# Kernel tuning notes

Hardware: AMD Instinct MI355X
Metric: run time of the kernel (lower is better)

Reference implementation:

```python
import jax, jax.numpy as jnp
import numpy as np

B, IN, HID, LAT, EH = 32768, 512, 2048, 128, 512
MID = max(HID // 2, LAT * 2)      # 1024
HALF = max(EH // 2, 4)            # 256
EPS = 1e-5
LN10 = float(np.log(10.0))


def setup_inputs() -> dict:
    key = jax.random.key(0)
    ks = jax.random.split(key, 24)
    r = lambda k, shp, s=0.02: (jax.random.normal(k, shp, dtype=jnp.float32) * s)
    d = {
        "x": jax.random.normal(ks[0], (B, IN), dtype=jnp.float32),
        "group_idx": jax.random.randint(ks[1], (B,), 0, 3),
        # encoder: Linear(IN,HID)+BN+ELU, Linear(HID,MID)+BN+ELU, Linear(MID,LAT)
        "e_w1": r(ks[2], (HID, IN)), "e_b1": jnp.zeros((HID,), jnp.float32),
        "e_g1": jnp.ones((HID,), jnp.float32), "e_be1": jnp.zeros((HID,), jnp.float32),
        "e_w2": r(ks[3], (MID, HID)), "e_b2": jnp.zeros((MID,), jnp.float32),
        "e_g2": jnp.ones((MID,), jnp.float32), "e_be2": jnp.zeros((MID,), jnp.float32),
        "e_w3": r(ks[4], (LAT, MID)), "e_b3": jnp.zeros((LAT,), jnp.float32),
        # shared: Linear(LAT+IN,HID)+BN+ELU, Linear(HID,MID)+BN+ELU
        "s_w1": r(ks[5], (HID, LAT + IN)), "s_b1": jnp.zeros((HID,), jnp.float32),
        "s_g1": jnp.ones((HID,), jnp.float32), "s_be1": jnp.zeros((HID,), jnp.float32),
        "s_w2": r(ks[6], (MID, HID)), "s_b2": jnp.zeros((MID,), jnp.float32),
        "s_g2": jnp.ones((MID,), jnp.float32), "s_be2": jnp.zeros((MID,), jnp.float32),
        # 3 expert heads, stacked on leading axis E=3
        "h_w1": r(ks[7], (3, EH, MID)), "h_b1": jnp.zeros((3, EH), jnp.float32),
        "h_w2": r(ks[8], (3, HALF, EH)), "h_b2": jnp.zeros((3, HALF), jnp.float32),
        "h_w3": r(ks[9], (3, HALF)), "h_b3": jnp.zeros((3,), jnp.float32),
    }
    return d


def _bn(h, g, b):
    # BatchNorm1d in training mode: batch mean, biased batch var
    m = jnp.mean(h, axis=0)
    v = jnp.var(h, axis=0)
    return (h - m) * (g / jnp.sqrt(v + EPS)) + b


def _elu(h):
    return jax.nn.elu(h)


def reference(x, group_idx,
              e_w1, e_b1, e_g1, e_be1, e_w2, e_b2, e_g2, e_be2, e_w3, e_b3,
              s_w1, s_b1, s_g1, s_be1, s_w2, s_b2, s_g2, s_be2,
              h_w1, h_b1, h_w2, h_b2, h_w3, h_b3):
    # encoder
    h = _elu(_bn(x @ e_w1.T + e_b1, e_g1, e_be1))
    h = _elu(_bn(h @ e_w2.T + e_b2, e_g2, e_be2))
    latent = h @ e_w3.T + e_b3                              # [B, LAT]
    # shared trunk
    z = jnp.concatenate([latent, x], axis=-1)               # [B, LAT+IN]
    h = _elu(_bn(z @ s_w1.T + s_b1, s_g1, s_be1))
    hidden = _elu(_bn(h @ s_w2.T + s_b2, s_g2, s_be2))      # [B, MID]
    # expert heads: compute all 3 (tiny vs trunk), then select per-row group
    t1 = _elu(jnp.einsum('bm,ehm->ebh', hidden, h_w1) + h_b1[:, None, :])   # [3,B,EH]
    t2 = _elu(jnp.einsum('ebh,efh->ebf', t1, h_w2) + h_b2[:, None, :])      # [3,B,HALF]
    pred_all = jnp.einsum('ebf,ef->eb', t2, h_w3) + h_b3[:, None]           # [3,B]
    pred_raw = jnp.take_along_axis(pred_all, group_idx[None, :], axis=0)[0] # [B]
    pred_log = -jax.nn.softplus(pred_raw)
    pred_prob = jnp.exp(pred_log * jnp.float32(LN10))       # 10 ** pred_log
    return pred_log, pred_prob
```

## Files before the change

kernel.cpp:

```cpp
#include <hip/hip_runtime.h>
#include <math.h>

#define B_    32768
#define LN10_ 2.302585092994046f
#define MT_H  264
#define NBLK  128

typedef __attribute__((ext_vector_type(8))) short short8;
typedef __attribute__((ext_vector_type(4))) float f32x4;

typedef const __attribute__((address_space(1))) void gvoid_t;
typedef __attribute__((address_space(3))) void svoid_t;

__device__ __forceinline__ void gl16(const void* g, void* l) {
  __builtin_amdgcn_global_load_lds((gvoid_t*)g, (svoid_t*)l, 16, 0, 0);
}

__device__ __forceinline__ float bf2f(unsigned int u) {
  union { unsigned int i; float f; } v; v.i = u << 16; return v.f;
}
__device__ __forceinline__ unsigned short f2bf(float f) {
  union { float f; unsigned int i; } v; v.f = f;
  unsigned int x = v.i;
  unsigned int r = x + 0x7FFFu + ((x >> 16) & 1u);
  return (unsigned short)(r >> 16);
}

#define HLF 8192

__global__ __launch_bounds__(512)
void gemm256(const unsigned short* __restrict__ A0_, int lda,
             const unsigned short* __restrict__ W0_, int ldw,
             unsigned short* __restrict__ C0, int ldc, int K,
             float* __restrict__ st, int Ntot) {
  __shared__ __align__(16) unsigned short lds[65536];
  const int t = threadIdx.x;
  const int nx = gridDim.x, ny = gridDim.y;
  const int f = blockIdx.y * nx + blockIdx.x;
  const int xcd = f & 7, g = f >> 3;
  const int gdiv = g / nx;
  const int mt = xcd * (ny >> 3) + gdiv;
  const int nt = g - gdiv * nx;
  const int mBase = mt * 256, nBase = nt * 256;
  const unsigned short* Ap = A0_ + (size_t)mBase * lda;
  const unsigned short* Wp = W0_ + (size_t)nBase * ldw;
  const int w = t >> 6, l = t & 63;
  const int wr = w >> 2, wc = w & 3;
  const int lm = l & 15, lg = l >> 4;

  const int rr = t >> 3;
  const int xc = ((t & 7) ^ (rr & 7)) << 3;
  const unsigned short* gA = Ap + (size_t)rr * lda + xc;
  const unsigned short* gB = Wp + (size_t)rr * ldw + xc;

#define SG(ptr, ld, rowoff, dst) \
    gl16((ptr) + (size_t)(rowoff) * (ld) + ko_, &lds[(dst) + t * 8])
#define STAGE_A0(tt) { const int d_=((tt)&1)<<15; const size_t ko_=(size_t)(tt)*64; \
    SG(gA,lda,0,d_);          SG(gA,lda,64,d_+4096); }
#define STAGE_A1(tt) { const int d_=((tt)&1)<<15; const size_t ko_=(size_t)(tt)*64; \
    SG(gA,lda,128,d_+8192);   SG(gA,lda,192,d_+12288); }
#define STAGE_B0(tt) { const int d_=((tt)&1)<<15; const size_t ko_=(size_t)(tt)*64; \
    SG(gB,ldw,0,d_+16384);    SG(gB,ldw,64,d_+20480); }
#define STAGE_B1(tt) { const int d_=((tt)&1)<<15; const size_t ko_=(size_t)(tt)*64; \
    SG(gB,ldw,128,d_+24576);  SG(gB,ldw,192,d_+28672); }

  const int cs0 = ((lg) ^ (l & 7)) << 3;
  const int cs1 = ((4 | lg) ^ (l & 7)) << 3;

  f32x4 acc[8][4];
#pragma unroll
  for (int i = 0; i < 8; ++i)
#pragma unroll
    for (int j = 0; j < 4; ++j) {
      f32x4 z4 = {0.f, 0.f, 0.f, 0.f};
      acc[i][j] = z4;
    }

  const int NT = K >> 6;
  STAGE_A0(0); STAGE_A1(0); STAGE_B0(0); STAGE_B1(0);
  asm volatile("s_waitcnt vmcnt(2)" ::: "memory");
  __builtin_amdgcn_s_barrier();

  short8 af[8], bq[4];
  for (int tt = 0; tt < NT; ++tt) {
    const int d = (tt & 1) << 15;
    const bool more = (tt + 1 < NT);
    const int abase = d + wr * HLF + lm * 64;
    const int bbase = d + 2 * HLF + (wc * 32 + lm) * 64;
#pragma unroll
    for (int i = 0; i < 8; ++i) af[i] = *(const short8*)&lds[abase + i * 1024 + cs0];
    bq[0] = *(const short8*)&lds[bbase + cs0];
    bq[1] = *(const short8*)&lds[bbase + 1024 + cs0];
    if (more) {
      STAGE_A0(tt + 1);
      asm volatile("s_waitcnt vmcnt(2)" ::: "memory");
    } else {
      asm volatile("s_waitcnt vmcnt(0)" ::: "memory");
    }
    __builtin_amdgcn_s_barrier();
    asm volatile("s_waitcnt lgkmcnt(0)" ::: "memory");
    __builtin_amdgcn_sched_barrier(0);
    __builtin_amdgcn_s_setprio(1);
#pragma unroll
    for (int i = 0; i < 8; ++i) {
      acc[i][0] = __builtin_amdgcn_mfma_f32_16x16x32_bf16(af[i], bq[0], acc[i][0], 0, 0, 0);
      acc[i][1] = __builtin_amdgcn_mfma_f32_16x16x32_bf16(af[i], bq[1], acc[i][1], 0, 0, 0);
    }
    __builtin_amdgcn_s_setprio(0);
    __builtin_amdgcn_s_barrier();
    bq[2] = *(const short8*)&lds[bbase + HLF + cs0];
    bq[3] = *(const short8*)&lds[bbase + HLF + 1024 + cs0];
    if (more) STAGE_A1(tt + 1);
    __builtin_amdgcn_s_barrier();
    asm volatile("s_waitcnt lgkmcnt(0)" ::: "memory");
    __builtin_amdgcn_sched_barrier(0);
    __builtin_amdgcn_s_setprio(1);
#pragma unroll
    for (int i = 0; i < 8; ++i) {
      acc[i][2] = __builtin_amdgcn_mfma_f32_16x16x32_bf16(af[i], bq[2], acc[i][2], 0, 0, 0);
      acc[i][3] = __builtin_amdgcn_mfma_f32_16x16x32_bf16(af[i], bq[3], acc[i][3], 0, 0, 0);
    }
    __builtin_amdgcn_s_setprio(0);
    __builtin_amdgcn_s_barrier();
#pragma unroll
    for (int i = 0; i < 8; ++i) af[i] = *(const short8*)&lds[abase + i * 1024 + cs1];
    bq[0] = *(const short8*)&lds[bbase + cs1];
    bq[1] = *(const short8*)&lds[bbase + 1024 + cs1];
    if (more) STAGE_B0(tt + 1);
    __builtin_amdgcn_s_barrier();
    asm volatile("s_waitcnt lgkmcnt(0)" ::: "memory");
    __builtin_amdgcn_sched_barrier(0);
    __builtin_amdgcn_s_setprio(1);
#pragma unroll
    for (int i = 0; i < 8; ++i) {
      acc[i][0] = __builtin_amdgcn_mfma_f32_16x16x32_bf16(af[i], bq[0], acc[i][0], 0, 0, 0);
      acc[i][1] = __builtin_amdgcn_mfma_f32_16x16x32_bf16(af[i], bq[1], acc[i][1], 0, 0, 0);
    }
    __builtin_amdgcn_s_setprio(0);
    __builtin_amdgcn_s_barrier();
    bq[2] = *(const short8*)&lds[bbase + HLF + cs1];
    bq[3] = *(const short8*)&lds[bbase + HLF + 1024 + cs1];
    if (more) {
      STAGE_B1(tt + 1);
      asm volatile("s_waitcnt vmcnt(2)" ::: "memory");
    }
    __builtin_amdgcn_s_barrier();
    asm volatile("s_waitcnt lgkmcnt(0)" ::: "memory");
    __builtin_amdgcn_sched_barrier(0);
    __builtin_amdgcn_s_setprio(1);
#pragma unroll
    for (int i = 0; i < 8; ++i) {
      acc[i][2] = __builtin_amdgcn_mfma_f32_16x16x32_bf16(af[i], bq[2], acc[i][2], 0, 0, 0);
      acc[i][3] = __builtin_amdgcn_mfma_f32_16x16x32_bf16(af[i], bq[3], acc[i][3], 0, 0, 0);
    }
    __builtin_amdgcn_s_setprio(0);
    __builtin_amdgcn_s_barrier();
  }

#pragma unroll
  for (int j = 0; j < 4; ++j) {
    int n = nBase + (j >> 1) * 128 + wc * 32 + (j & 1) * 16 + lm;
    float s1 = 0.f, q1 = 0.f;
#pragma unroll
    for (int i = 0; i < 8; ++i) {
      int m0 = mBase + wr * 128 + i * 16 + lg * 4;
#pragma unroll
      for (int r = 0; r < 4; ++r) {
        float v = acc[i][j][r];
        s1 += v; q1 += v * v;
        C0[(size_t)(m0 + r) * ldc + n] = f2bf(v);
      }
    }
    s1 += __shfl_xor(s1, 16, 64); s1 += __shfl_xor(s1, 32, 64);
    q1 += __shfl_xor(q1, 16, 64); q1 += __shfl_xor(q1, 32, 64);
    if (lg == 0) { atomicAdd(&st[n], s1); atomicAdd(&st[Ntot + n], q1); }
  }
}
#undef SG
#undef STAGE_A0
#undef STAGE_A1
#undef STAGE_B0
#undef STAGE_B1

__global__ __launch_bounds__(256)
void gemm_bt(const unsigned short* __restrict__ A0, int lda,
             const unsigned short* __restrict__ W0, int ldw,
             unsigned short* __restrict__ C0, int ldc,
             int K, const float* __restrict__ bias0, int elu,
             float* __restrict__ st, int Ntot,
             long eA, long eW, long eC, int eBias,
             const int* __restrict__ texp) {
  __shared__ __align__(16) unsigned short lA[128 * 64];
  __shared__ __align__(16) unsigned short lB[128 * 64];
  const int t = threadIdx.x;
  const int nx = gridDim.x, ny = gridDim.y;
  const int f = blockIdx.y * nx + blockIdx.x;
  const int xcd = f & 7, g = f >> 3;
  const int gdiv = g / nx;
  const int mt = xcd * (ny >> 3) + gdiv;
  const int nt = g - gdiv * nx;
  const int mBase = mt * 128;
  const int nBase = nt * 128;
  int e = texp ? texp[mt] : (int)blockIdx.z;
  if (e < 0) return;
  const unsigned short* A = A0 + (size_t)e * eA;
  const unsigned short* W = W0 + (size_t)e * eW;
  unsigned short* C = C0 + (size_t)e * eC;
  const float* bias = bias0 ? (bias0 + (size_t)e * eBias) : nullptr;
  const unsigned short* Ap = A + (size_t)mBase * lda;
  const unsigned short* Wp = W + (size_t)nBase * ldw;
  const int w = t >> 6, l = t & 63;
  const int wr = (w >> 1) * 64, wc = (w & 1) * 64;
  const int lm = l & 15, lg = l >> 4;

  f32x4 acc[4][4];
#pragma unroll
  for (int i = 0; i < 4; ++i)
#pragma unroll
    for (int j = 0; j < 4; ++j) {
      f32x4 z4 = {0.f, 0.f, 0.f, 0.f};
      acc[i][j] = z4;
    }

  for (int k0 = 0; k0 < K; k0 += 64) {
    __syncthreads();
#pragma unroll
    for (int it = 0; it < 4; ++it) {
      int chunk = it * 256 + t;
      int row = chunk >> 3, sc = chunk & 7;
      int gc = (sc ^ (row & 7)) << 3;
      gl16(Ap + (size_t)row * lda + k0 + gc, &lA[chunk * 8]);
      gl16(Wp + (size_t)row * ldw + k0 + gc, &lB[chunk * 8]);
    }
    __syncthreads();
#pragma unroll
    for (int kk = 0; kk < 64; kk += 32) {
      short8 af[4], bfr[4];
#pragma unroll
      for (int i = 0; i < 4; ++i) {
        int ar = wr + i * 16 + lm;
        int ac = (kk >> 3) + lg;
        af[i] = *(const short8*)&lA[ar * 64 + ((ac ^ (ar & 7)) << 3)];
      }
#pragma unroll
      for (int j = 0; j < 4; ++j) {
        int br = wc + j * 16 + lm;
        int bc = (kk >> 3) + lg;
        bfr[j] = *(const short8*)&lB[br * 64 + ((bc ^ (br & 7)) << 3)];
      }
#pragma unroll
      for (int i = 0; i < 4; ++i)
#pragma unroll
        for (int j = 0; j < 4; ++j)
          acc[i][j] = __builtin_amdgcn_mfma_f32_16x16x32_bf16(af[i], bfr[j], acc[i][j], 0, 0, 0);
    }
  }

#pragma unroll
  for (int j = 0; j < 4; ++j) {
    int n = nBase + wc + j * 16 + lm;
    float bj = bias ? bias[n] : 0.f;
    float s = 0.f, q = 0.f;
#pragma unroll
    for (int i = 0; i < 4; ++i) {
      int m0 = mBase + wr + i * 16 + lg * 4;
#pragma unroll
      for (int r = 0; r < 4; ++r) {
        float v = acc[i][j][r] + bj;
        if (elu) v = v > 0.f ? v : expm1f(v);
        s += v; q += v * v;
        C[(size_t)(m0 + r) * ldc + n] = f2bf(v);
      }
    }
    if (st) {
      s += __shfl_xor(s, 16, 64); s += __shfl_xor(s, 32, 64);
      q += __shfl_xor(q, 16, 64); q += __shfl_xor(q, 32, 64);
      if (lg == 0) { atomicAdd(&st[n], s); atomicAdd(&st[Ntot + n], q); }
    }
  }
}

__global__ void bn_apply(unsigned short* __restrict__ Y, const float* __restrict__ st,
                         const float* __restrict__ gam, const float* __restrict__ bet,
                         int N, float invB) {
  size_t i = (size_t)blockIdx.x * blockDim.x + threadIdx.x;
  size_t base = i * 8;
  int col = (int)(base & (size_t)(N - 1));
  float a8[8], b8[8];
#pragma unroll
  for (int k = 0; k < 8; ++k) {
    int c = col + k;
    float m = st[c] * invB;
    float var = st[N + c] * invB - m * m;
    float av = gam[c] * rsqrtf(var + 1e-5f);
    a8[k] = av;
    b8[k] = bet[c] - m * av;
  }
  uint4 u = *(uint4*)&Y[base];
  unsigned int uu[4] = {u.x, u.y, u.z, u.w};
  unsigned int oo[4];
#pragma unroll
  for (int k = 0; k < 4; ++k) {
    float vlo = bf2f(uu[k] & 0xFFFFu);
    float vhi = bf2f(uu[k] >> 16);
    float flo = a8[2 * k] * vlo + b8[2 * k];
    float fhi = a8[2 * k + 1] * vhi + b8[2 * k + 1];
    flo = flo > 0.f ? flo : expm1f(flo);
    fhi = fhi > 0.f ? fhi : expm1f(fhi);
    oo[k] = (unsigned int)f2bf(flo) | ((unsigned int)f2bf(fhi) << 16);
  }
  uint4 o = {oo[0], oo[1], oo[2], oo[3]};
  *(uint4*)&Y[base] = o;
}

__global__ void cast_all(const float* __restrict__ e1, const float* __restrict__ e2,
                         const float* __restrict__ e3, const float* __restrict__ s1,
                         const float* __restrict__ s2, const float* __restrict__ h1,
                         const float* __restrict__ h2, unsigned short* __restrict__ dst) {
  int i4 = blockIdx.x * 256 + threadIdx.x;
  const float* src;
  int rel;
  if (i4 < 786432) {
    if (i4 < 262144) { src = e1; rel = i4; }
    else             { src = e2; rel = i4 - 262144; }
  } else if (i4 < 1146880) {
    if (i4 < 819200) { src = e3; rel = i4 - 786432; }
    else             { src = s1; rel = i4 - 819200; }
  } else if (i4 < 2064384) {
    if (i4 < 1671168) { src = s2; rel = i4 - 1146880; }
    else              { src = h1; rel = i4 - 1671168; }
  } else { src = h2; rel = i4 - 2064384; }
  float4 v = ((const float4*)src)[rel];
  ushort4 o = {f2bf(v.x), f2bf(v.y), f2bf(v.z), f2bf(v.w)};
  ((ushort4*)dst)[i4] = o;
}

__global__ void cast_x(const float* __restrict__ x, unsigned short* __restrict__ z) {
  int i = blockIdx.x * blockDim.x + threadIdx.x;
  int b = i >> 7;
  int c = (i & 127) << 2;
  float4 v = *(const float4*)&x[(size_t)b * 512 + c];
  ushort4 o = {f2bf(v.x), f2bf(v.y), f2bf(v.z), f2bf(v.w)};
  *(ushort4*)&z[(size_t)b * 640 + 128 + c] = o;
}

__global__ void hist_blocks(const int* __restrict__ gidx, int* __restrict__ bcnt) {
  int blk = blockIdx.x;
  int i = blk * 256 + threadIdx.x;
  int e = gidx[i];
  int l = threadIdx.x & 63, w = threadIdx.x >> 6;
  __shared__ int wc[4][3];
  unsigned long long m0 = __ballot(e == 0);
  unsigned long long m1 = __ballot(e == 1);
  unsigned long long m2 = __ballot(e == 2);
  if (l == 0) { wc[w][0] = __popcll(m0); wc[w][1] = __popcll(m1); wc[w][2] = __popcll(m2); }
  __syncthreads();
  if (threadIdx.x < 3)
    bcnt[blk * 3 + threadIdx.x] = wc[0][threadIdx.x] + wc[1][threadIdx.x] +
                                  wc[2][threadIdx.x] + wc[3][threadIdx.x];
}

__global__ void scan_plan(const int* __restrict__ bcnt, int* __restrict__ boff,
                          int* __restrict__ vend, int* __restrict__ texp) {
  __shared__ int sp[4];
  __shared__ int cnt[3];
  int t = threadIdx.x;
  if (t < 3) {
    int s = 0;
    for (int b = 0; b < NBLK; ++b) s += bcnt[b * 3 + t];
    cnt[t] = s;
  }
  __syncthreads();
  if (t == 0) {
    int p = 0;
    for (int e = 0; e < 3; ++e) {
      sp[e] = p; vend[e] = p + cnt[e];
      p += ((cnt[e] + 127) >> 7) << 7;
    }
    sp[3] = p;
  }
  __syncthreads();
  if (t < 3) {
    int run = sp[t];
    for (int b = 0; b < NBLK; ++b) { boff[b * 3 + t] = run; run += bcnt[b * 3 + t]; }
  }
  if (t < MT_H) {
    int r0 = t << 7, e = -1;
    for (int k = 0; k < 3; ++k)
      if (r0 >= sp[k] && r0 < sp[k + 1]) e = k;
    texp[t] = e;
  }
}

__global__ void scatter2(const int* __restrict__ gidx, const int* __restrict__ boff,
                         int* __restrict__ perm) {
  int blk = blockIdx.x;
  int i = blk * 256 + threadIdx.x;
  int e = gidx[i];
  int l = threadIdx.x & 63, w = threadIdx.x >> 6;
  __shared__ int wc[4][3];
  unsigned long long m0 = __ballot(e == 0);
  unsigned long long m1 = __ballot(e == 1);
  unsigned long long m2 = __ballot(e == 2);
  if (l == 0) { wc[w][0] = __popcll(m0); wc[w][1] = __popcll(m1); wc[w][2] = __popcll(m2); }
  __syncthreads();
  unsigned long long me = (e == 0) ? m0 : ((e == 1) ? m1 : m2);
  int rank = __popcll(me & ((1ull << l) - 1ull));
  int woff = 0;
  for (int ww = 0; ww < w; ++ww) woff += wc[ww][e];
  perm[boff[blk * 3 + e] + woff + rank] = i;
}

__global__ void gather_h(const unsigned short* __restrict__ hid, const int* __restrict__ perm,
                         const int* __restrict__ texp, const int* __restrict__ vend,
                         unsigned short* __restrict__ ht) {
  int idx = blockIdx.x * 256 + threadIdx.x;
  int p = idx >> 7, c8 = (idx & 127) << 3;
  int e = texp[p >> 7];
  uint4 v = {0u, 0u, 0u, 0u};
  if (e >= 0 && p < vend[e]) {
    int src = perm[p];
    v = *(const uint4*)&hid[(size_t)src * 1024 + c8];
  }
  *(uint4*)&ht[(size_t)p * 1024 + c8] = v;
}

__global__ void final_pred(const unsigned short* __restrict__ t2, const int* __restrict__ perm,
                           const int* __restrict__ texp, const int* __restrict__ vend,
                           const float* __restrict__ w3, const float* __restrict__ b3,
                           float* __restrict__ out) {
  int p = blockIdx.x * 4 + (threadIdx.x >> 6);
  int l = threadIdx.x & 63;
  int e = texp[p >> 7];
  if (e < 0 || p >= vend[e]) return;
  ushort4 u = *(const ushort4*)&t2[(size_t)p * 256 + l * 4];
  float4 wv = *(const float4*)&w3[e * 256 + l * 4];
  float sum = bf2f(u.x) * wv.x + bf2f(u.y) * wv.y + bf2f(u.z) * wv.z + bf2f(u.w) * wv.w;
#pragma unroll
  for (int off = 32; off; off >>= 1) sum += __shfl_down(sum, off, 64);
  if (l == 0) {
    int orig = perm[p];
    float xr = sum + b3[e];
    float sp = (xr > 0.f) ? (xr + log1pf(expf(-xr))) : log1pf(expf(xr));
    float pl = -sp;
    out[orig] = pl;
    out[B_ + orig] = expf(pl * LN10_);
  }
}

extern "C" void kernel_launch(void* const* d_in, const int* in_sizes, int n_in,
                              void* d_out, int out_size, void* d_ws, size_t ws_size,
                              hipStream_t stream) {
  const float* x    = (const float*)d_in[0];
  const int*   gidx = (const int*)d_in[1];
  const float* e_w1 = (const float*)d_in[2];
  const float* e_g1 = (const float*)d_in[4];
  const float* e_be1= (const float*)d_in[5];
  const float* e_w2 = (const float*)d_in[6];
  const float* e_g2 = (const float*)d_in[8];
  const float* e_be2= (const float*)d_in[9];
  const float* e_w3 = (const float*)d_in[10];
  const float* e_b3 = (const float*)d_in[11];
  const float* s_w1 = (const float*)d_in[12];
  const float* s_g1 = (const float*)d_in[14];
  const float* s_be1= (const float*)d_in[15];
  const float* s_w2 = (const float*)d_in[16];
  const float* s_g2 = (const float*)d_in[18];
  const float* s_be2= (const float*)d_in[19];
  const float* h_w1 = (const float*)d_in[20];
  const float* h_b1 = (const float*)d_in[21];
  const float* h_w2 = (const float*)d_in[22];
  const float* h_b2 = (const float*)d_in[23];
  const float* h_w3 = (const float*)d_in[24];
  const float* h_b3 = (const float*)d_in[25];
  float* out = (float*)d_out;

  char* ws = (char*)d_ws;
  size_t off = 0;
  auto alloc = [&](size_t bytes) -> char* {
    char* p = ws + off;
    off += (bytes + 255) & ~(size_t)255;
    return p;
  };
  unsigned short* wb_e1 = (unsigned short*)alloc((size_t)2048 * 512 * 2);
  unsigned short* wb_e2 = (unsigned short*)alloc((size_t)1024 * 2048 * 2);
  unsigned short* wb_e3 = (unsigned short*)alloc((size_t)128 * 1024 * 2);
  unsigned short* wb_s1 = (unsigned short*)alloc((size_t)2048 * 640 * 2);
  unsigned short* wb_s2 = (unsigned short*)alloc((size_t)1024 * 2048 * 2);
  unsigned short* wb_h1 = (unsigned short*)alloc((size_t)3 * 512 * 1024 * 2);
  unsigned short* wb_h2 = (unsigned short*)alloc((size_t)3 * 256 * 512 * 2);
  unsigned short* z     = (unsigned short*)alloc((size_t)B_ * 640 * 2);
  unsigned short* bufA  = (unsigned short*)alloc((size_t)B_ * 2048 * 2);
  unsigned short* bufB  = (unsigned short*)alloc((size_t)B_ * 1024 * 2);
  float* st = (float*)alloc(12288 * sizeof(float));
  float* st0 = st;
  float* st1 = st + 4096;
  float* st2 = st + 6144;
  float* st3 = st + 10240;
  int* bcnt = (int*)alloc(NBLK * 3 * sizeof(int));
  int* boff = (int*)alloc(NBLK * 3 * sizeof(int));
  int* vend = (int*)alloc(3 * sizeof(int));
  int* texp = (int*)alloc(MT_H * sizeof(int));
  int* perm = (int*)alloc((size_t)MT_H * 128 * sizeof(int));
  unsigned short* ht  = bufA;
  unsigned short* t1p = bufA + (size_t)MT_H * 128 * 1024;
  unsigned short* t2p = z;

  cast_all<<<8448, 256, 0, stream>>>(e_w1, e_w2, e_w3, s_w1, s_w2, h_w1, h_w2, wb_e1);
  cast_x<<<(B_ * 128) / 256, 256, 0, stream>>>(x, z);
  hipMemsetAsync(st, 0, 12288 * sizeof(float), stream);
  hist_blocks<<<NBLK, 256, 0, stream>>>(gidx, bcnt);
  scan_plan<<<1, 512, 0, stream>>>(bcnt, boff, vend, texp);
  scatter2<<<NBLK, 256, 0, stream>>>(gidx, boff, perm);

  gemm256<<<dim3(8, 128), 512, 0, stream>>>(z + 128, 640, wb_e1, 512, bufA, 2048, 512,
                                            st0, 2048);
  bn_apply<<<B_, 256, 0, stream>>>(bufA, st0, e_g1, e_be1, 2048, 1.0f / B_);
  gemm256<<<dim3(4, 128), 512, 0, stream>>>(bufA, 2048, wb_e2, 2048, bufB, 1024, 2048,
                                            st1, 1024);
  bn_apply<<<B_ / 2, 256, 0, stream>>>(bufB, st1, e_g2, e_be2, 1024, 1.0f / B_);
  gemm_bt<<<dim3(1, 256), 256, 0, stream>>>(bufB, 1024, wb_e3, 1024, z, 640, 1024,
                                            e_b3, 0, nullptr, 0, 0, 0, 0, 0, nullptr);
  gemm256<<<dim3(8, 128), 512, 0, stream>>>(z, 640, wb_s1, 640, bufA, 2048, 640,
                                            st2, 2048);
  bn_apply<<<B_, 256, 0, stream>>>(bufA, st2, s_g1, s_be1, 2048, 1.0f / B_);
  gemm256<<<dim3(4, 128), 512, 0, stream>>>(bufA, 2048, wb_s2, 2048, bufB, 1024, 2048,
                                            st3, 1024);
  bn_apply<<<B_ / 2, 256, 0, stream>>>(bufB, st3, s_g2, s_be2, 1024, 1.0f / B_);

  gather_h<<<(MT_H * 128 * 128) / 256, 256, 0, stream>>>(bufB, perm, texp, vend, ht);

  gemm_bt<<<dim3(4, MT_H), 256, 0, stream>>>(ht, 1024, wb_h1, 1024, t1p, 512, 1024,
                                             h_b1, 1, nullptr, 0,
                                             0, (long)512 * 1024, 0, 512, texp);
  gemm_bt<<<dim3(2, MT_H), 256, 0, stream>>>(t1p, 512, wb_h2, 512, t2p, 256, 512,
                                             h_b2, 1, nullptr, 0,
                                             0, (long)256 * 512, 0, 256, texp);

  final_pred<<<(MT_H * 128) / 4, 256, 0, stream>>>(t2p, perm, texp, vend, h_w3, h_b3, out);
}
```

Baseline: 1.006 ms.

## Restructure GEMM main loop into quadrant schedule with fewer barriers

After: 1.044 ms. +3.8%, slower.

```diff
diff --git a/kernel.cpp b/kernel.cpp
--- a/kernel.cpp
+++ b/kernel.cpp
@@ -26,7 +26,6 @@
   return (unsigned short)(r >> 16);
 }
 
-#define HLF 8192
 
 __global__ __launch_bounds__(512)
 void gemm256(const unsigned short* __restrict__ A0_, int lda,
@@ -56,16 +55,18 @@
 #define SG(ptr, ld, rowoff, dst) \
     gl16((ptr) + (size_t)(rowoff) * (ld) + ko_, &lds[(dst) + t * 8])
 #define STAGE_A0(tt) { const int d_=((tt)&1)<<15; const size_t ko_=(size_t)(tt)*64; \
-    SG(gA,lda,0,d_);          SG(gA,lda,64,d_+4096); }
+    SG(gA,lda,0,d_);           SG(gA,lda,64,d_+4096); }
 #define STAGE_A1(tt) { const int d_=((tt)&1)<<15; const size_t ko_=(size_t)(tt)*64; \
-    SG(gA,lda,128,d_+8192);   SG(gA,lda,192,d_+12288); }
+    SG(gA,lda,128,d_+8192);    SG(gA,lda,192,d_+12288); }
 #define STAGE_B0(tt) { const int d_=((tt)&1)<<15; const size_t ko_=(size_t)(tt)*64; \
-    SG(gB,ldw,0,d_+16384);    SG(gB,ldw,64,d_+20480); }
+    SG(gB,ldw,0,d_+16384);     SG(gB,ldw,64,d_+20480); }
 #define STAGE_B1(tt) { const int d_=((tt)&1)<<15; const size_t ko_=(size_t)(tt)*64; \
-    SG(gB,ldw,128,d_+24576);  SG(gB,ldw,192,d_+28672); }
+    SG(gB,ldw,128,d_+24576);   SG(gB,ldw,192,d_+28672); }
 
   const int cs0 = ((lg) ^ (l & 7)) << 3;
   const int cs1 = ((4 | lg) ^ (l & 7)) << 3;
+  const int ab = (wr * 128 + lm) * 64;
+  const int bb = 16384 + (wc * 64 + lm) * 64;
 
   f32x4 acc[8][4];
 #pragma unroll
@@ -77,89 +78,93 @@
     }
 
   const int NT = K >> 6;
-  STAGE_A0(0); STAGE_A1(0); STAGE_B0(0); STAGE_B1(0);
+  STAGE_A0(0); STAGE_A1(0); STAGE_B0(0); STAGE_B1(0); STAGE_A0(1);
   asm volatile("s_waitcnt vmcnt(2)" ::: "memory");
   __builtin_amdgcn_s_barrier();
-
-  short8 af[8], bq[4];
+  __builtin_amdgcn_sched_barrier(0);
+
+  short8 af[4][2], bc0[2][2], bc1[2][2];
   for (int tt = 0; tt < NT; ++tt) {
     const int d = (tt & 1) << 15;
-    const bool more = (tt + 1 < NT);
-    const int abase = d + wr * HLF + lm * 64;
-    const int bbase = d + 2 * HLF + (wc * 32 + lm) * 64;
-#pragma unroll
-    for (int i = 0; i < 8; ++i) af[i] = *(const short8*)&lds[abase + i * 1024 + cs0];
-    bq[0] = *(const short8*)&lds[bbase + cs0];
-    bq[1] = *(const short8*)&lds[bbase + 1024 + cs0];
-    if (more) {
-      STAGE_A0(tt + 1);
-      asm volatile("s_waitcnt vmcnt(2)" ::: "memory");
-    } else {
-      asm volatile("s_waitcnt vmcnt(0)" ::: "memory");
-    }
-    __builtin_amdgcn_s_barrier();
+    const bool s1ok = (tt + 1 < NT), s2ok = (tt + 2 < NT);
+#pragma unroll
+    for (int fi = 0; fi < 4; ++fi) {
+      af[fi][0] = *(const short8*)&lds[d + ab + fi * 1024 + cs0];
+      af[fi][1] = *(const short8*)&lds[d + ab + fi * 1024 + cs1];
+    }
+#pragma unroll
+    for (int fj = 0; fj < 2; ++fj) {
+      bc0[fj][0] = *(const short8*)&lds[d + bb + fj * 1024 + cs0];
+      bc0[fj][1] = *(const short8*)&lds[d + bb + fj * 1024 + cs1];
+    }
+    if (s1ok) STAGE_A1(tt + 1);
     asm volatile("s_waitcnt lgkmcnt(0)" ::: "memory");
     __builtin_amdgcn_sched_barrier(0);
     __builtin_amdgcn_s_setprio(1);
 #pragma unroll
-    for (int i = 0; i < 8; ++i) {
-      acc[i][0] = __builtin_amdgcn_mfma_f32_16x16x32_bf16(af[i], bq[0], acc[i][0], 0, 0, 0);
-      acc[i][1] = __builtin_amdgcn_mfma_f32_16x16x32_bf16(af[i], bq[1], acc[i][1], 0, 0, 0);
-    }
+    for (int fi = 0; fi < 4; ++fi)
+#pragma unroll
+      for (int fj = 0; fj < 2; ++fj) {
+        acc[fi][fj] = __builtin_amdgcn_mfma_f32_16x16x32_bf16(af[fi][0], bc0[fj][0], acc[fi][fj], 0, 0, 0);
+        acc[fi][fj] = __builtin_amdgcn_mfma_f32_16x16x32_bf16(af[fi][1], bc0[fj][1], acc[fi][fj], 0, 0, 0);
+      }
     __builtin_amdgcn_s_setprio(0);
-    __builtin_amdgcn_s_barrier();
-    bq[2] = *(const short8*)&lds[bbase + HLF + cs0];
-    bq[3] = *(const short8*)&lds[bbase + HLF + 1024 + cs0];
-    if (more) STAGE_A1(tt + 1);
-    __builtin_amdgcn_s_barrier();
+#pragma unroll
+    for (int fj = 0; fj < 2; ++fj) {
+      bc1[fj][0] = *(const short8*)&lds[d + bb + 2048 + fj * 1024 + cs0];
+      bc1[fj][1] = *(const short8*)&lds[d + bb + 2048 + fj * 1024 + cs1];
+    }
+    if (s1ok) STAGE_B0(tt + 1);
     asm volatile("s_waitcnt lgkmcnt(0)" ::: "memory");
     __builtin_amdgcn_sched_barrier(0);
     __builtin_amdgcn_s_setprio(1);
 #pragma unroll
-    for (int i = 0; i < 8; ++i) {
-      acc[i][2] = __builtin_amdgcn_mfma_f32_16x16x32_bf16(af[i], bq[2], acc[i][2], 0, 0, 0);
-      acc[i][3] = __builtin_amdgcn_mfma_f32_16x16x32_bf16(af[i], bq[3], acc[i][3], 0, 0, 0);
-    }
+    for (int fi = 0; fi < 4; ++fi)
+#pragma unroll
+      for (int fj = 0; fj < 2; ++fj) {
+        acc[fi][2 + fj] = __builtin_amdgcn_mfma_f32_16x16x32_bf16(af[fi][0], bc1[fj][0], acc[fi][2 + fj], 0, 0, 0);
+        acc[fi][2 + fj] = __builtin_amdgcn_mfma_f32_16x16x32_bf16(af[fi][1], bc1[fj][1], acc[fi][2 + fj], 0, 0, 0);
+      }
     __builtin_amdgcn_s_setprio(0);
-    __builtin_amdgcn_s_barrier();
-#pragma unroll
-    for (int i = 0; i < 8; ++i) af[i] = *(const short8*)&lds[abase + i * 1024 + cs1];
-    bq[0] = *(const short8*)&lds[bbase + cs1];
-    bq[1] = *(const short8*)&lds[bbase + 1024 + cs1];
-    if (more) STAGE_B0(tt + 1);
-    __builtin_amdgcn_s_barrier();
+#pragma unroll
+    for (int fi = 0; fi < 4; ++fi) {
+      af[fi][0] = *(const short8*)&lds[d + ab + 4096 + fi * 1024 + cs0];
+      af[fi][1] = *(const short8*)&lds[d + ab + 4096 + fi * 1024 + cs1];
+    }
+    if (s1ok) STAGE_B1(tt + 1);
     asm volatile("s_waitcnt lgkmcnt(0)" ::: "memory");
     __builtin_amdgcn_sched_barrier(0);
     __builtin_amdgcn_s_setprio(1);
 #pragma unroll
-    for (int i = 0; i < 8; ++i) {
-      acc[i][0] = __builtin_amdgcn_mfma_f32_16x16x32_bf16(af[i], bq[0], acc[i][0], 0, 0, 0);
-      acc[i][1] = __builtin_amdgcn_mfma_f32_16x16x32_bf16(af[i], bq[1], acc[i][1], 0, 0, 0);
-    }
+    for (int fi = 0; fi < 4; ++fi)
+#pragma unroll
+      for (int fj = 0; fj < 2; ++fj) {
+        acc[4 + fi][fj] = __builtin_amdgcn_mfma_f32_16x16x32_bf16(af[fi][0], bc0[fj][0], acc[4 + fi][fj], 0, 0, 0);
+        acc[4 + fi][fj] = __builtin_amdgcn_mfma_f32_16x16x32_bf16(af[fi][1], bc0[fj][1], acc[4 + fi][fj], 0, 0, 0);
+      }
     __builtin_amdgcn_s_setprio(0);
     __builtin_amdgcn_s_barrier();
-    bq[2] = *(const short8*)&lds[bbase + HLF + cs1];
-    bq[3] = *(const short8*)&lds[bbase + HLF + 1024 + cs1];
-    if (more) {
-      STAGE_B1(tt + 1);
-      asm volatile("s_waitcnt vmcnt(2)" ::: "memory");
-    }
-    __builtin_amdgcn_s_barrier();
-    asm volatile("s_waitcnt lgkmcnt(0)" ::: "memory");
-    __builtin_amdgcn_sched_barrier(0);
+    if (s2ok) STAGE_A0(tt + 2);
     __builtin_amdgcn_s_setprio(1);
 #pragma unroll
-    for (int i = 0; i < 8; ++i) {
-      acc[i][2] = __builtin_amdgcn_mfma_f32_16x16x32_bf16(af[i], bq[2], acc[i][2], 0, 0, 0);
-      acc[i][3] = __builtin_amdgcn_mfma_f32_16x16x32_bf16(af[i], bq[3], acc[i][3], 0, 0, 0);
-    }
+    for (int fi = 0; fi < 4; ++fi)
+#pragma unroll
+      for (int fj = 0; fj < 2; ++fj) {
+        acc[4 + fi][2 + fj] = __builtin_amdgcn_mfma_f32_16x16x32_bf16(af[fi][0], bc1[fj][0], acc[4 + fi][2 + fj], 0, 0, 0);
+        acc[4 + fi][2 + fj] = __builtin_amdgcn_mfma_f32_16x16x32_bf16(af[fi][1], bc1[fj][1], acc[4 + fi][2 + fj], 0, 0, 0);
+      }
     __builtin_amdgcn_s_setprio(0);
-    __builtin_amdgcn_s_barrier();
+    if (s1ok) {
+      if (s2ok) { asm volatile("s_waitcnt vmcnt(2)" ::: "memory"); }
+      else      { asm volatile("s_waitcnt vmcnt(0)" ::: "memory"); }
+      __builtin_amdgcn_s_barrier();
+      __builtin_amdgcn_sched_barrier(0);
+    }
   }
 
 #pragma unroll
   for (int j = 0; j < 4; ++j) {
-    int n = nBase + (j >> 1) * 128 + wc * 32 + (j & 1) * 16 + lm;
+    int n = nBase + wc * 64 + j * 16 + lm;
     float s1 = 0.f, q1 = 0.f;
 #pragma unroll
     for (int i = 0; i < 8; ++i) {
```

## Add single-barrier 256-tile GEMM variant and move expert heads to 256 tiles

Applied to the files above, without the earlier changes.

Measured after the change: 1.061 ms. 5.5% more time.

```diff
diff --git a/kernel.cpp b/kernel.cpp
--- a/kernel.cpp
+++ b/kernel.cpp
@@ -3,7 +3,8 @@
 
 #define B_    32768
 #define LN10_ 2.302585092994046f
-#define MT_H  264
+#define MT256 136
+#define MT_H  272
 #define NBLK  128
 
 typedef __attribute__((ext_vector_type(8))) short short8;
@@ -26,13 +27,147 @@
   return (unsigned short)(r >> 16);
 }
 
+#define TLA 16384
 #define HLF 8192
 
 __global__ __launch_bounds__(512)
-void gemm256(const unsigned short* __restrict__ A0_, int lda,
-             const unsigned short* __restrict__ W0_, int ldw,
-             unsigned short* __restrict__ C0, int ldc, int K,
-             float* __restrict__ st, int Ntot) {
+void gemm256a(const unsigned short* __restrict__ A0_, int lda,
+              const unsigned short* __restrict__ W0_, int ldw,
+              unsigned short* __restrict__ C0, int ldc, int K,
+              const float* __restrict__ bias0, int elu,
+              float* __restrict__ st, int Ntot,
+              long eW, int eBias, const int* __restrict__ texp) {
+  __shared__ __align__(16) unsigned short lds[4 * TLA];
+  const int t = threadIdx.x;
+  const int nx = gridDim.x, ny = gridDim.y;
+  const int f = blockIdx.y * nx + blockIdx.x;
+  const int xcd = f & 7, g = f >> 3;
+  const int gdiv = g / nx;
+  const int mt = xcd * (ny >> 3) + gdiv;
+  const int nt = g - gdiv * nx;
+  const int mBase = mt * 256, nBase = nt * 256;
+  const int e = texp ? texp[mt * 2] : 0;
+  if (e < 0) return;
+  const unsigned short* Ap = A0_ + (size_t)mBase * lda;
+  const unsigned short* Wp = W0_ + (size_t)e * eW + (size_t)nBase * ldw;
+  const float* bias = bias0 ? (bias0 + (size_t)e * eBias) : nullptr;
+  const int w = t >> 6, l = t & 63;
+  const int wr = w >> 2, wc = w & 3;
+  const int lm = l & 15, lg = l >> 4;
+
+  const int rr = t >> 3;
+  const int xc = ((t & 7) ^ (rr & 7)) << 3;
+  const unsigned short* gA = Ap + (size_t)rr * lda + xc;
+  const unsigned short* gB = Wp + (size_t)rr * ldw + xc;
+
+#define SGA(ptr, ld, rowoff, dst) \
+    gl16((ptr) + (size_t)(rowoff) * (ld) + ko_, &lds[(dst) + t * 8])
+#define ASTAGE_A(tt) { const int d_=((tt)&1)*2*TLA; const size_t ko_=(size_t)(tt)*64; \
+    SGA(gA,lda,0,d_);            SGA(gA,lda,64,d_+4096);   \
+    SGA(gA,lda,128,d_+8192);     SGA(gA,lda,192,d_+12288); }
+#define ASTAGE_B(tt) { const int d_=((tt)&1)*2*TLA+TLA; const size_t ko_=(size_t)(tt)*64; \
+    SGA(gB,ldw,0,d_);            SGA(gB,ldw,64,d_+4096);   \
+    SGA(gB,ldw,128,d_+8192);     SGA(gB,ldw,192,d_+12288); }
+
+  const int cs0 = ((lg) ^ (l & 7)) << 3;
+  const int cs1 = ((4 | lg) ^ (l & 7)) << 3;
+
+  f32x4 acc[8][4];
+#pragma unroll
+  for (int i = 0; i < 8; ++i)
+#pragma unroll
+    for (int j = 0; j < 4; ++j) {
+      f32x4 z4 = {0.f, 0.f, 0.f, 0.f};
+      acc[i][j] = z4;
+    }
+
+  const int NT = K >> 6;
+  ASTAGE_A(0); ASTAGE_B(0);
+
+  for (int tt = 0; tt < NT; ++tt) {
+    asm volatile("s_waitcnt vmcnt(0)" ::: "memory");
+    __builtin_amdgcn_s_barrier();
+    __builtin_amdgcn_sched_barrier(0);
+    const int d = (tt & 1) * 2 * TLA;
+    const bool more = (tt + 1 < NT);
+    if (more) ASTAGE_A(tt + 1);
+    {
+      short8 af[8], bq[4];
+#pragma unroll
+      for (int i = 0; i < 8; ++i) {
+        int arow = wr * 128 + i * 16 + lm;
+        af[i] = *(const short8*)&lds[d + arow * 64 + cs0];
+      }
+#pragma unroll
+      for (int j = 0; j < 4; ++j) {
+        int brow = wc * 64 + j * 16 + lm;
+        bq[j] = *(const short8*)&lds[d + TLA + brow * 64 + cs0];
+      }
+      __builtin_amdgcn_s_setprio(1);
+#pragma unroll
+      for (int i = 0; i < 8; ++i)
+#pragma unroll
+        for (int j = 0; j < 4; ++j)
+          acc[i][j] = __builtin_amdgcn_mfma_f32_16x16x32_bf16(af[i], bq[j], acc[i][j], 0, 0, 0);
+      __builtin_amdgcn_s_setprio(0);
+    }
+    if (more) ASTAGE_B(tt + 1);
+    {
+      short8 af[8], bq[4];
+#pragma unroll
+      for (int i = 0; i < 8; ++i) {
+        int arow = wr * 128 + i * 16 + lm;
+        af[i] = *(const short8*)&lds[d + arow * 64 + cs1];
+      }
+#pragma unroll
+      for (int j = 0; j < 4; ++j) {
+        int brow = wc * 64 + j * 16 + lm;
+        bq[j] = *(const short8*)&lds[d + TLA + brow * 64 + cs1];
+      }
+      __builtin_amdgcn_s_setprio(1);
+#pragma unroll
+      for (int i = 0; i < 8; ++i)
+#pragma unroll
+        for (int j = 0; j < 4; ++j)
+          acc[i][j] = __builtin_amdgcn_mfma_f32_16x16x32_bf16(af[i], bq[j], acc[i][j], 0, 0, 0);
+      __builtin_amdgcn_s_setprio(0);
+    }
+  }
+
+#pragma unroll
+  for (int j = 0; j < 4; ++j) {
+    int n = nBase + wc * 64 + j * 16 + lm;
+    float bj = bias ? bias[n - nBase + (nt ? nBase : 0)] : 0.f;
+    bj = bias ? bias[n] : 0.f;
+    float s1 = 0.f, q1 = 0.f;
+#pragma unroll
+    for (int i = 0; i < 8; ++i) {
+      int m0 = mBase + wr * 128 + i * 16 + lg * 4;
+#pragma unroll
+      for (int r = 0; r < 4; ++r) {
+        float v = acc[i][j][r] + bj;
+        if (elu) v = v > 0.f ? v : expm1f(v);
+        s1 += v; q1 += v * v;
+        C0[(size_t)(m0 + r) * ldc + n] = f2bf(v);
+      }
+    }
+    if (st) {
+      s1 += __shfl_xor(s1, 16, 64); s1 += __shfl_xor(s1, 32, 64);
+      q1 += __shfl_xor(q1, 16, 64); q1 += __shfl_xor(q1, 32, 64);
+      if (lg == 0) { atomicAdd(&st[n], s1); atomicAdd(&st[Ntot + n], q1); }
+    }
+  }
+}
+#undef ASTAGE_A
+#undef ASTAGE_B
+
+__global__ __launch_bounds__(512)
+void gemm256b(const unsigned short* __restrict__ A0_, int lda,
+              const unsigned short* __restrict__ W0_, int ldw,
+              unsigned short* __restrict__ C0, int ldc, int K,
+              const float* __restrict__ bias0, int elu,
+              float* __restrict__ st, int Ntot,
+              long eW, int eBias, const int* __restrict__ texp) {
   __shared__ __align__(16) unsigned short lds[65536];
   const int t = threadIdx.x;
   const int nx = gridDim.x, ny = gridDim.y;
@@ -42,8 +177,11 @@
   const int mt = xcd * (ny >> 3) + gdiv;
   const int nt = g - gdiv * nx;
   const int mBase = mt * 256, nBase = nt * 256;
+  const int e = texp ? texp[mt * 2] : 0;
+  if (e < 0) return;
   const unsigned short* Ap = A0_ + (size_t)mBase * lda;
-  const unsigned short* Wp = W0_ + (size_t)nBase * ldw;
+  const unsigned short* Wp = W0_ + (size_t)e * eW + (size_t)nBase * ldw;
+  const float* bias = bias0 ? (bias0 + (size_t)e * eBias) : nullptr;
   const int w = t >> 6, l = t & 63;
   const int wr = w >> 2, wc = w & 3;
   const int lm = l & 15, lg = l >> 4;
@@ -53,16 +191,16 @@
   const unsigned short* gA = Ap + (size_t)rr * lda + xc;
   const unsigned short* gB = Wp + (size_t)rr * ldw + xc;
 
-#define SG(ptr, ld, rowoff, dst) \
+#define SGB(ptr, ld, rowoff, dst) \
     gl16((ptr) + (size_t)(rowoff) * (ld) + ko_, &lds[(dst) + t * 8])
-#define STAGE_A0(tt) { const int d_=((tt)&1)<<15; const size_t ko_=(size_t)(tt)*64; \
-    SG(gA,lda,0,d_);          SG(gA,lda,64,d_+4096); }
-#define STAGE_A1(tt) { const int d_=((tt)&1)<<15; const size_t ko_=(size_t)(tt)*64; \
-    SG(gA,lda,128,d_+8192);   SG(gA,lda,192,d_+12288); }
-#define STAGE_B0(tt) { const int d_=((tt)&1)<<15; const size_t ko_=(size_t)(tt)*64; \
-    SG(gB,ldw,0,d_+16384);    SG(gB,ldw,64,d_+20480); }
-#define STAGE_B1(tt) { const int d_=((tt)&1)<<15; const size_t ko_=(size_t)(tt)*64; \
-    SG(gB,ldw,128,d_+24576);  SG(gB,ldw,192,d_+28672); }
+#define BSTAGE_A0(tt) { const int d_=((tt)&1)<<15; const size_t ko_=(size_t)(tt)*64; \
+    SGB(gA,lda,0,d_);          SGB(gA,lda,64,d_+4096); }
+#define BSTAGE_A1(tt) { const int d_=((tt)&1)<<15; const size_t ko_=(size_t)(tt)*64; \
+    SGB(gA,lda,128,d_+8192);   SGB(gA,lda,192,d_+12288); }
+#define BSTAGE_B0(tt) { const int d_=((tt)&1)<<15; const size_t ko_=(size_t)(tt)*64; \
+    SGB(gB,ldw,0,d_+16384);    SGB(gB,ldw,64,d_+20480); }
+#define BSTAGE_B1(tt) { const int d_=((tt)&1)<<15; const size_t ko_=(size_t)(tt)*64; \
+    SGB(gB,ldw,128,d_+24576);  SGB(gB,ldw,192,d_+28672); }
 
   const int cs0 = ((lg) ^ (l & 7)) << 3;
   const int cs1 = ((4 | lg) ^ (l & 7)) << 3;
@@ -77,7 +215,7 @@
     }
 
   const int NT = K >> 6;
-  STAGE_A0(0); STAGE_A1(0); STAGE_B0(0); STAGE_B1(0);
+  BSTAGE_A0(0); BSTAGE_A1(0); BSTAGE_B0(0); BSTAGE_B1(0);
   asm volatile("s_waitcnt vmcnt(2)" ::: "memory");
   __builtin_amdgcn_s_barrier();
 
@@ -92,7 +230,7 @@
     bq[0] = *(const short8*)&lds[bbase + cs0];
     bq[1] = *(const short8*)&lds[bbase + 1024 + cs0];
     if (more) {
-      STAGE_A0(tt + 1);
+      BSTAGE_A0(tt + 1);
       asm volatile("s_waitcnt vmcnt(2)" ::: "memory");
     } else {
       asm volatile("s_waitcnt vmcnt(0)" ::: "memory");
@@ -110,7 +248,7 @@
     __builtin_amdgcn_s_barrier();
     bq[2] = *(const short8*)&lds[bbase + HLF + cs0];
     bq[3] = *(const short8*)&lds[bbase + HLF + 1024 + cs0];
-    if (more) STAGE_A1(tt + 1);
+    if (more) BSTAGE_A1(tt + 1);
     __builtin_amdgcn_s_barrier();
     asm volatile("s_waitcnt lgkmcnt(0)" ::: "memory");
     __builtin_amdgcn_sched_barrier(0);
@@ -126,7 +264,7 @@
     for (int i = 0; i < 8; ++i) af[i] = *(const short8*)&lds[abase + i * 1024 + cs1];
     bq[0] = *(const short8*)&lds[bbase + cs1];
     bq[1] = *(const short8*)&lds[bbase + 1024 + cs1];
-    if (more) STAGE_B0(tt + 1);
+    if (more) BSTAGE_B0(tt + 1);
     __builtin_amdgcn_s_barrier();
     asm volatile("s_waitcnt lgkmcnt(0)" ::: "memory");
     __builtin_amdgcn_sched_barrier(0);
@@ -141,7 +279,7 @@
     bq[2] = *(const short8*)&lds[bbase + HLF + cs1];
     bq[3] = *(const short8*)&lds[bbase + HLF + 1024 + cs1];
     if (more) {
-      STAGE_B1(tt + 1);
+      BSTAGE_B1(tt + 1);
       asm volatile("s_waitcnt vmcnt(2)" ::: "memory");
     }
     __builtin_amdgcn_s_barrier();
@@ -160,27 +298,31 @@
 #pragma unroll
   for (int j = 0; j < 4; ++j) {
     int n = nBase + (j >> 1) * 128 + wc * 32 + (j & 1) * 16 + lm;
+    float bj = bias ? bias[n] : 0.f;
     float s1 = 0.f, q1 = 0.f;
 #pragma unroll
     for (int i = 0; i < 8; ++i) {
       int m0 = mBase + wr * 128 + i * 16 + lg * 4;
 #pragma unroll
       for (int r = 0; r < 4; ++r) {
-        float v = acc[i][j][r];
+        float v = acc[i][j][r] + bj;
+        if (elu) v = v > 0.f ? v : expm1f(v);
         s1 += v; q1 += v * v;
         C0[(size_t)(m0 + r) * ldc + n] = f2bf(v);
       }
     }
-    s1 += __shfl_xor(s1, 16, 64); s1 += __shfl_xor(s1, 32, 64);
-    q1 += __shfl_xor(q1, 16, 64); q1 += __shfl_xor(q1, 32, 64);
-    if (lg == 0) { atomicAdd(&st[n], s1); atomicAdd(&st[Ntot + n], q1); }
-  }
-}
-#undef SG
-#undef STAGE_A0
-#undef STAGE_A1
-#undef STAGE_B0
-#undef STAGE_B1
+    if (st) {
+      s1 += __shfl_xor(s1, 16, 64); s1 += __shfl_xor(s1, 32, 64);
+      q1 += __shfl_xor(q1, 16, 64); q1 += __shfl_xor(q1, 32, 64);
+      if (lg == 0) { atomicAdd(&st[n], s1); atomicAdd(&st[Ntot + n], q1); }
+    }
+  }
+}
+#undef SGB
+#undef BSTAGE_A0
+#undef BSTAGE_A1
+#undef BSTAGE_B0
+#undef BSTAGE_B1
 
 __global__ __launch_bounds__(256)
 void gemm_bt(const unsigned short* __restrict__ A0, int lda,
@@ -375,7 +517,7 @@
     int p = 0;
     for (int e = 0; e < 3; ++e) {
       sp[e] = p; vend[e] = p + cnt[e];
-      p += ((cnt[e] + 127) >> 7) << 7;
+      p += ((cnt[e] + 255) >> 8) << 8;
     }
     sp[3] = p;
   }
@@ -513,29 +655,29 @@
   scan_plan<<<1, 512, 0, stream>>>(bcnt, boff, vend, texp);
   scatter2<<<NBLK, 256, 0, stream>>>(gidx, boff, perm);
 
-  gemm256<<<dim3(8, 128), 512, 0, stream>>>(z + 128, 640, wb_e1, 512, bufA, 2048, 512,
-                                            st0, 2048);
+  gemm256b<<<dim3(8, 128), 512, 0, stream>>>(z + 128, 640, wb_e1, 512, bufA, 2048, 512,
+                                             nullptr, 0, st0, 2048, 0, 0, nullptr);
   bn_apply<<<B_, 256, 0, stream>>>(bufA, st0, e_g1, e_be1, 2048, 1.0f / B_);
-  gemm256<<<dim3(4, 128), 512, 0, stream>>>(bufA, 2048, wb_e2, 2048, bufB, 1024, 2048,
-                                            st1, 1024);
+  gemm256a<<<dim3(4, 128), 512, 0, stream>>>(bufA, 2048, wb_e2, 2048, bufB, 1024, 2048,
+                                             nullptr, 0, st1, 1024, 0, 0, nullptr);
   bn_apply<<<B_ / 2, 256, 0, stream>>>(bufB, st1, e_g2, e_be2, 1024, 1.0f / B_);
   gemm_bt<<<dim3(1, 256), 256, 0, stream>>>(bufB, 1024, wb_e3, 1024, z, 640, 1024,
                                             e_b3, 0, nullptr, 0, 0, 0, 0, 0, nullptr);
-  gemm256<<<dim3(8, 128), 512, 0, stream>>>(z, 640, wb_s1, 640, bufA, 2048, 640,
-                                            st2, 2048);
+  gemm256b<<<dim3(8, 128), 512, 0, stream>>>(z, 640, wb_s1, 640, bufA, 2048, 640,
+                                             nullptr, 0, st2, 2048, 0, 0, nullptr);
   bn_apply<<<B_, 256, 0, stream>>>(bufA, st2, s_g1, s_be1, 2048, 1.0f / B_);
-  gemm256<<<dim3(4, 128), 512, 0, stream>>>(bufA, 2048, wb_s2, 2048, bufB, 1024, 2048,
-                                            st3, 1024);
+  gemm256a<<<dim3(4, 128), 512, 0, stream>>>(bufA, 2048, wb_s2, 2048, bufB, 1024, 2048,
+                                             nullptr, 0, st3, 1024, 0, 0, nullptr);
   bn_apply<<<B_ / 2, 256, 0, stream>>>(bufB, st3, s_g2, s_be2, 1024, 1.0f / B_);
 
   gather_h<<<(MT_H * 128 * 128) / 256, 256, 0, stream>>>(bufB, perm, texp, vend, ht);
 
-  gemm_bt<<<dim3(4, MT_H), 256, 0, stream>>>(ht, 1024, wb_h1, 1024, t1p, 512, 1024,
-                                             h_b1, 1, nullptr, 0,
-                                             0, (long)512 * 1024, 0, 512, texp);
-  gemm_bt<<<dim3(2, MT_H), 256, 0, stream>>>(t1p, 512, wb_h2, 512, t2p, 256, 512,
-                                             h_b2, 1, nullptr, 0,
-                                             0, (long)256 * 512, 0, 256, texp);
+  gemm256b<<<dim3(2, MT256), 512, 0, stream>>>(ht, 1024, wb_h1, 1024, t1p, 512, 1024,
+                                               h_b1, 1, nullptr, 0,
+                                               (long)512 * 1024, 512, texp);
+  gemm256b<<<dim3(1, MT256), 512, 0, stream>>>(t1p, 512, wb_h2, 512, t2p, 256, 512,
+                                               h_b2, 1, nullptr, 0,
+                                               (long)256 * 512, 256, texp);
 
   final_pred<<<(MT_H * 128) / 4, 256, 0, stream>>>(t2p, perm, texp, vend, h_w3, h_b3, out);
 }
```
